# Kernel optimization log

Measured on AMD Instinct MI355X. Metric: run time of the kernel, lower is better.

Reference implementation:

```python
import jax, jax.numpy as jnp
import numpy as np

B, N, C = 4, 2304, 256
H = 8                      # num_heads
D = C // H                 # head_dim = 32
SCALE = D ** -0.5
H_DS, W_DS = 48, 48
UP = 2                     # spatial_down_ratio
EPS = 1e-5


def setup_inputs() -> dict:
    key = jax.random.key(0)
    ks = jax.random.split(key, 16)
    g = lambda k, shape, s: (jax.random.normal(k, shape, dtype=jnp.float32) * s)
    return {
        "x1": g(ks[0], (B, N, C), 1.0),
        "x2": g(ks[1], (B, N, C), 1.0),
        # attention projections (torch Linear convention: [out, in], no bias)
        "q1_w": g(ks[2], (C, C), C ** -0.5),
        "kv1_w": g(ks[3], (2 * C, C), C ** -0.5),
        "q2_w": g(ks[4], (C, C), C ** -0.5),
        "kv2_w": g(ks[5], (2 * C, C), C ** -0.5),
        # per-head scalar biases
        "beta12": jnp.full((H,), 0.2, dtype=jnp.float32),
        "beta21": jnp.full((H,), 0.1, dtype=jnp.float32),
        # output projections
        "p1_w": g(ks[6], (C, C), (2.0 / C) ** 0.5),
        "p1_b": g(ks[7], (C,), 1e-2),
        "p2_w": g(ks[8], (C, C), (2.0 / C) ** 0.5),
        "p2_b": g(ks[9], (C,), 1e-2),
        # LayerNorm affine params
        "g1": jnp.ones((C,), dtype=jnp.float32),
        "b1": jnp.zeros((C,), dtype=jnp.float32),
        "g2": jnp.ones((C,), dtype=jnp.float32),
        "b2": jnp.zeros((C,), dtype=jnp.float32),
    }


def _heads(x):
    # [B,N,C] -> [B,H,N,D]
    return x.reshape(B, N, H, D).transpose(0, 2, 1, 3)


def _merge(x):
    # [B,H,N,D] -> [B,N,C]
    return x.transpose(0, 2, 1, 3).reshape(B, N, C)


def _cross_attn(q, k, v, beta):
    # scores: [B,H,N,N] with per-head scalar bias
    s = jnp.einsum("bhqd,bhkd->bhqk", q, k) * SCALE + beta[None, :, None, None]
    a = jax.nn.softmax(s, axis=-1)
    return jnp.einsum("bhqk,bhkd->bhqd", a, v)


def _layernorm(x, g, b):
    mu = jnp.mean(x, axis=-1, keepdims=True)
    var = jnp.var(x, axis=-1, keepdims=True)
    return (x - mu) * jax.lax.rsqrt(var + EPS) * g + b


def _forward(x1, x2, q1_w, kv1_w, q2_w, kv2_w, beta12, beta21,
             p1_w, p1_b, p2_w, p2_b, g1, b1, g2, b2):
    q1 = _heads(x1 @ q1_w.T)
    kv1 = x1 @ kv1_w.T          # [B,N,2C]
    k1, v1 = _heads(kv1[..., :C]), _heads(kv1[..., C:])
    q2 = _heads(x2 @ q2_w.T)
    kv2 = x2 @ kv2_w.T
    k2, v2 = _heads(kv2[..., :C]), _heads(kv2[..., C:])

    o1 = _merge(_cross_attn(q1, k2, v2, beta12))   # x1 attends to x2
    o2 = _merge(_cross_attn(q2, k1, v1, beta21))   # x2 attends to x1

    y1 = _layernorm(jax.nn.relu(o1 @ p1_w.T + p1_b), g1, b1)
    y2 = _layernorm(jax.nn.relu(o2 @ p2_w.T + p2_b), g2, b2)

    # [B,N,C] -> [B,C,H_ds,W_ds]
    y1 = y1.transpose(0, 2, 1).reshape(B, C, H_DS, W_DS)
    y2 = y2.transpose(0, 2, 1).reshape(B, C, H_DS, W_DS)

    # bilinear upsample x2, align_corners=False (half-pixel == jax.image default)
    out_shape = (B, C, H_DS * UP, W_DS * UP)
    y1 = jax.image.resize(y1, out_shape, method="bilinear")
    y2 = jax.image.resize(y2, out_shape, method="bilinear")
    return y1, y2


def reference(x1, x2, q1_w, kv1_w, q2_w, kv2_w, beta12, beta21,
              p1_w, p1_b, p2_w, p2_b, g1, b1, g2, b2):
    return _forward(x1, x2, q1_w, kv1_w, q2_w, kv2_w, beta12, beta21,
                    p1_w, p1_b, p2_w, p2_b, g1, b1, g2, b2)
```

## Files before the change

kernel.cpp:

```cpp
#include <hip/hip_runtime.h>
#include <math.h>


typedef __attribute__((ext_vector_type(8))) short short8;
typedef __attribute__((ext_vector_type(4))) float f32x4;
typedef __attribute__((ext_vector_type(16))) float f32x16;
typedef __attribute__((ext_vector_type(2))) unsigned uint32x2;

#define MFMA16(a, b, c) __builtin_amdgcn_mfma_f32_16x16x32_bf16((a), (b), (c), 0, 0, 0)
#define MFMA32(a, b, c) __builtin_amdgcn_mfma_f32_32x32x16_bf16((a), (b), (c), 0, 0, 0)

__device__ __forceinline__ float bf2f(ushort u) {
    union { unsigned u; float f; } x; x.u = ((unsigned)u) << 16; return x.f;
}
__device__ __forceinline__ ushort f2bf(float f) {
    union { float f; unsigned u; } x; x.f = f;
    unsigned u = x.u;
    return (ushort)((u + 0x7fffu + ((u >> 16) & 1u)) >> 16);
}
__device__ __forceinline__ unsigned cvt_pk_bf16(float a, float b) {
    unsigned r;
    asm("v_cvt_pk_bf16_f32 %0, %1, %2" : "=v"(r) : "v"(a), "v"(b));
    return r;
}
__device__ __forceinline__ float fast_ex2(float x) {
    float r;
    asm("v_exp_f32 %0, %1" : "=v"(r) : "v"(x));
    return r;
}
__device__ __forceinline__ void plswap(unsigned &a, unsigned &b) {
    uint32x2 r = __builtin_amdgcn_permlane32_swap(a, b, false, false);
    a = r[0]; b = r[1];
}

__global__ void sniff_kernel(const ushort* __restrict__ x, int* __restrict__ flag)
{
    int lane = threadIdx.x;
    ushort u = x[lane * 2];
    int e = (u >> 7) & 0xFF;
    int outlier = (e < 100 || e > 135) ? 1 : 0;
    unsigned long long m = __ballot(outlier);
    if (lane == 0) *flag = (__popcll(m) >= 16) ? 1 : 0;
}

__global__ __launch_bounds__(256) void convert_params(
    const void* s0, const void* s1, const void* s2, const void* s3,
    const void* s4, const void* s5, const void* s6, const void* s7,
    const void* s8, const void* s9, const void* s10, const void* s11,
    ushort* __restrict__ dst, const int* __restrict__ flag)
{
    int idx = blockIdx.x * 256 + threadIdx.x;
    if (idx >= 525824) return;
    const void* src; int off;
    if      (idx < 65536)  { src = s0;  off = idx; }
    else if (idx < 196608) { src = s1;  off = idx - 65536; }
    else if (idx < 262144) { src = s2;  off = idx - 196608; }
    else if (idx < 393216) { src = s3;  off = idx - 262144; }
    else if (idx < 458752) { src = s4;  off = idx - 393216; }
    else if (idx < 524288) { src = s5;  off = idx - 458752; }
    else if (idx < 524544) { src = s6;  off = idx - 524288; }
    else if (idx < 524800) { src = s7;  off = idx - 524544; }
    else if (idx < 525056) { src = s8;  off = idx - 524800; }
    else if (idx < 525312) { src = s9;  off = idx - 525056; }
    else if (idx < 525568) { src = s10; off = idx - 525312; }
    else                   { src = s11; off = idx - 525568; }
    ushort v = (*flag) ? f2bf(((const float*)src)[off])
                       : ((const ushort*)src)[off];
    dst[idx] = v;
}

__global__ __launch_bounds__(256) void convert_x(
    const void* __restrict__ x1, const void* __restrict__ x2,
    ushort* __restrict__ o1, ushort* __restrict__ o2,
    const int* __restrict__ flag)
{
    int idx = blockIdx.x * 256 + threadIdx.x;
    int which = idx >= 294912;
    int off = (which ? idx - 294912 : idx) * 8;
    const void* src = which ? x2 : x1;
    ushort* dst = which ? o2 : o1;
    if (*flag) {
        const float* p = (const float*)src + off;
        float4 a = *(const float4*)p;
        float4 c = *(const float4*)(p + 4);
        uint4 u;
        u.x = cvt_pk_bf16(a.x, a.y);
        u.y = cvt_pk_bf16(a.z, a.w);
        u.z = cvt_pk_bf16(c.x, c.y);
        u.w = cvt_pk_bf16(c.z, c.w);
        *(uint4*)(dst + off) = u;
    } else {
        *(uint4*)(dst + off) = *(const uint4*)((const ushort*)src + off);
    }
}

__global__ __launch_bounds__(256) void gemm_bt(
    const void* __restrict__ Ain, const ushort* __restrict__ W,
    ushort* __restrict__ C, const ushort* __restrict__ bias,
    int M, int N, int K, int relu, const int* __restrict__ dflag, int a_ext,
    int mode, ushort* __restrict__ Kh, ushort* __restrict__ Vt,
    const ushort* __restrict__ W2, const ushort* __restrict__ bias2,
    ushort* __restrict__ Kh2, ushort* __restrict__ Vt2, int mhalf)
{
    __shared__ __align__(16) ushort As[64][40];
    __shared__ __align__(16) ushort Ws[64][40];

    const int m0 = blockIdx.x * 64;
    const int n0 = blockIdx.y * 64;
    const int tid = threadIdx.x;
    const int w = tid >> 6;
    const int lane = tid & 63;
    const int lm = lane & 15;
    const int quad = lane >> 4;
    const int a32 = a_ext ? *dflag : 0;

    const int side = (mhalf && m0 >= mhalf) ? 1 : 0;
    const ushort* Wu = side ? W2 : W;
    const ushort* bu = side ? bias2 : bias;
    ushort* Khu = side ? Kh2 : Kh;
    ushort* Vtu = side ? Vt2 : Vt;

    const f32x4 Z4 = {0.f, 0.f, 0.f, 0.f};
    f32x4 acc[4];
    for (int j = 0; j < 4; j++) acc[j] = Z4;

    const ushort* A16 = (const ushort*)Ain;
    const float*  A32 = (const float*)Ain;
    const int row = tid >> 2, off = (tid & 3) * 8;

    for (int k0 = 0; k0 < K; k0 += 32) {
        __syncthreads();
        if (a32) {
            const float* p0 = A32 + (size_t)(m0 + row) * K + k0 + off;
            float4 f0 = *(const float4*)p0;
            float4 f1 = *(const float4*)(p0 + 4);
            uint4 t0;
            t0.x = cvt_pk_bf16(f0.x, f0.y);
            t0.y = cvt_pk_bf16(f0.z, f0.w);
            t0.z = cvt_pk_bf16(f1.x, f1.y);
            t0.w = cvt_pk_bf16(f1.z, f1.w);
            *(uint4*)&As[row][off] = t0;
        } else {
            *(uint4*)&As[row][off] =
                *(const uint4*)(A16 + (size_t)(m0 + row) * K + k0 + off);
        }
        *(uint4*)&Ws[row][off] =
            *(const uint4*)(Wu + (size_t)(n0 + row) * K + k0 + off);
        __syncthreads();

        short8 af = *(const short8*)&As[w * 16 + lm][quad * 8];
        for (int nt = 0; nt < 4; nt++) {
            short8 wf = *(const short8*)&Ws[nt * 16 + lm][quad * 8];
            acc[nt] = MFMA16(af, wf, acc[nt]);
        }
    }

    const int grow = m0 + w * 16 + quad * 4;
    const int grel = grow - (side ? mhalf : 0);
    if (mode == 1) {
        const float QSC = 0.17677669529663687f * 1.4426950408889634f;
        int bb = grel / 2304;
        int tok = grel - bb * 2304;
        for (int nt = 0; nt < 4; nt++) {
            int col = n0 + nt * 16 + lm;
            if (col < 256) {
                for (int r = 0; r < 4; r++)
                    C[(size_t)(grow + r) * 256 + col] = f2bf(acc[nt][r] * QSC);
            } else if (col < 512) {
                int c2 = col - 256, hh = c2 >> 5, d = c2 & 31;
                size_t kb = ((size_t)(bb * 8 + hh) * 72 + (tok >> 5)) * 1024
                          + (size_t)(d >> 4) * 512 + (size_t)(d & 15);
                for (int r = 0; r < 4; r++)
                    Khu[kb + (size_t)((tok + r) & 31) * 16] = f2bf(acc[nt][r]);
            } else {
                int c2 = col - 512, hh = c2 >> 5, d = c2 & 31;
                size_t vb = ((size_t)(bb * 8 + hh) * 144 + (tok >> 4)) * 512
                          + (size_t)d * 16 + (size_t)(tok & 15);
                uint2 o;
                o.x = cvt_pk_bf16(acc[nt][0], acc[nt][1]);
                o.y = cvt_pk_bf16(acc[nt][2], acc[nt][3]);
                *(uint2*)&Vtu[vb] = o;
            }
        }
    } else {
        for (int nt = 0; nt < 4; nt++) {
            int col = n0 + nt * 16 + lm;
            float bv = bu ? bf2f(bu[col]) : 0.f;
            for (int r = 0; r < 4; r++) {
                float v = acc[nt][r] + bv;
                if (relu) v = fmaxf(v, 0.f);
                C[(size_t)(grow + r) * N + col] = f2bf(v);
            }
        }
    }
}

__global__ __launch_bounds__(128) void attn_kernel(
    const ushort* __restrict__ Qa, const ushort* __restrict__ Kha,
    const ushort* __restrict__ Vta, ushort* __restrict__ Oa,
    const ushort* __restrict__ Qb, const ushort* __restrict__ Khb2,
    const ushort* __restrict__ Vtb2, ushort* __restrict__ Ob)
{
    const int sid = blockIdx.x;
    const int qb = blockIdx.y;
    const int side = sid >> 5;
    const int bh = sid & 31;
    const ushort* Q  = side ? Qb   : Qa;
    const ushort* Kh = side ? Khb2 : Kha;
    const ushort* Vt = side ? Vtb2 : Vta;
    ushort* O        = side ? Ob   : Oa;

    const int b = bh >> 3, h = bh & 7;
    const int tid = threadIdx.x;
    const int w = tid >> 6, lane = tid & 63;
    const int l31 = lane & 31, hl = lane >> 5;

    const int qrow0 = qb * 128 + w * 64 + l31;
    const int qrow1 = qrow0 + 32;
    const ushort* qp0 = Q + ((size_t)b * 2304 + qrow0) * 256 + h * 32 + hl * 8;
    const ushort* qp1 = Q + ((size_t)b * 2304 + qrow1) * 256 + h * 32 + hl * 8;
    const short8 qf0a = *(const short8*)qp0;
    const short8 qf1a = *(const short8*)(qp0 + 16);
    const short8 qf0b = *(const short8*)qp1;
    const short8 qf1b = *(const short8*)(qp1 + 16);

    f32x16 oa, ob;
    #pragma unroll
    for (int i = 0; i < 16; i++) { oa[i] = 0.f; ob[i] = 0.f; }
    const f32x16 Z16 = oa;
    float la = 0.f, lb = 0.f;

    const ushort* kp0 = Kh + (size_t)bh * 73728 + l31 * 16 + hl * 8;
    const ushort* vp0 = Vt + (size_t)bh * 73728 + l31 * 16 + hl * 8;

#define LOADT(kf0v, kf1v, vf0v, vf1v, t) { \
    const ushort* _kp = kp0 + (size_t)(t) * 1024; \
    kf0v = *(const short8*)_kp; \
    kf1v = *(const short8*)(_kp + 512); \
    const ushort* _vp = vp0 + (size_t)(t) * 1024; \
    vf0v = *(const short8*)_vp; \
    vf1v = *(const short8*)(_vp + 512); \
}
#define QSET(kf0v, kf1v, vf0v, vf1v, qf0v, qf1v, oacc, lacc) { \
    f32x16 s = MFMA32(kf0v, qf0v, Z16); \
    s = MFMA32(kf1v, qf1v, s); \
    float p[16]; \
    _Pragma("unroll") \
    for (int i = 0; i < 16; i++) p[i] = fast_ex2(s[i]); \
    lacc += (((p[0] + p[1]) + (p[2] + p[3])) + ((p[4] + p[5]) + (p[6] + p[7]))) \
          + (((p[8] + p[9]) + (p[10] + p[11])) + ((p[12] + p[13]) + (p[14] + p[15]))); \
    unsigned c0 = cvt_pk_bf16(p[0],  p[1]); \
    unsigned c1 = cvt_pk_bf16(p[2],  p[3]); \
    unsigned c2 = cvt_pk_bf16(p[4],  p[5]); \
    unsigned c3 = cvt_pk_bf16(p[6],  p[7]); \
    unsigned c4 = cvt_pk_bf16(p[8],  p[9]); \
    unsigned c5 = cvt_pk_bf16(p[10], p[11]); \
    unsigned c6 = cvt_pk_bf16(p[12], p[13]); \
    unsigned c7 = cvt_pk_bf16(p[14], p[15]); \
    plswap(c0, c2); plswap(c1, c3); plswap(c4, c6); plswap(c5, c7); \
    union { unsigned u[4]; short8 s8; } pA, pB; \
    pA.u[0] = c0; pA.u[1] = c1; pA.u[2] = c2; pA.u[3] = c3; \
    pB.u[0] = c4; pB.u[1] = c5; pB.u[2] = c6; pB.u[3] = c7; \
    oacc = MFMA32(vf0v, pA.s8, oacc); \
    oacc = MFMA32(vf1v, pB.s8, oacc); \
}
#define COMP(kf0v, kf1v, vf0v, vf1v) { \
    QSET(kf0v, kf1v, vf0v, vf1v, qf0a, qf1a, oa, la); \
    QSET(kf0v, kf1v, vf0v, vf1v, qf0b, qf1b, ob, lb); \
}

    short8 kA0, kA1, vA0, vA1;
    short8 kB0, kB1, vB0, vB1;

    LOADT(kA0, kA1, vA0, vA1, 0);
    LOADT(kB0, kB1, vB0, vB1, 1);

    for (int t = 0; t < 72; t += 2) {
        COMP(kA0, kA1, vA0, vA1);
        { int ta = t + 2 < 72 ? t + 2 : 70; LOADT(kA0, kA1, vA0, vA1, ta); }
        COMP(kB0, kB1, vB0, vB1);
        { int tb = t + 3 < 72 ? t + 3 : 71; LOADT(kB0, kB1, vB0, vB1, tb); }
    }
#undef LOADT
#undef QSET
#undef COMP

    la += __shfl_xor(la, 32, 64);
    lb += __shfl_xor(lb, 32, 64);
    float ra = 1.f / la, rb = 1.f / lb;
    ushort* op0 = O + ((size_t)b * 2304 + qrow0) * 256 + h * 32 + hl * 4;
    ushort* op1 = O + ((size_t)b * 2304 + qrow1) * 256 + h * 32 + hl * 4;
    #pragma unroll
    for (int g = 0; g < 4; g++) {
        uint2 o;
        o.x = cvt_pk_bf16(oa[4 * g] * ra, oa[4 * g + 1] * ra);
        o.y = cvt_pk_bf16(oa[4 * g + 2] * ra, oa[4 * g + 3] * ra);
        *(uint2*)(op0 + 8 * g) = o;
        uint2 o2;
        o2.x = cvt_pk_bf16(ob[4 * g] * rb, ob[4 * g + 1] * rb);
        o2.y = cvt_pk_bf16(ob[4 * g + 2] * rb, ob[4 * g + 3] * rb);
        *(uint2*)(op1 + 8 * g) = o2;
    }
}

__global__ __launch_bounds__(256) void lnt_kernel(
    const ushort* __restrict__ Z, const ushort* __restrict__ G1,
    const ushort* __restrict__ B1, const ushort* __restrict__ G2,
    const ushort* __restrict__ B2, ushort* __restrict__ Yt)
{
    __shared__ ushort T[256][72];

    const int tid = threadIdx.x;
    const int tok0 = blockIdx.x * 32;
    const int half = (tok0 >= 9216) ? 1 : 0;
    const int tr = tok0 - half * 9216;
    const int bb = tr / 2304;
    const int tokb = tr - bb * 2304;

    const int tok_l = tid >> 3;
    const int cq = tid & 7;

    const ushort* zp = Z + ((size_t)(tok0 + tok_l)) * 256 + cq * 32;
    uint dd[16];
    for (int i = 0; i < 4; i++) {
        uint4 v = *(const uint4*)(zp + i * 8);
        dd[i * 4 + 0] = v.x; dd[i * 4 + 1] = v.y;
        dd[i * 4 + 2] = v.z; dd[i * 4 + 3] = v.w;
    }
    float s = 0.f, q = 0.f;
    for (int e = 0; e < 16; e++) {
        float x0 = bf2f((ushort)dd[e]);
        float x1 = bf2f((ushort)(dd[e] >> 16));
        s += x0 + x1;
        q += x0 * x0 + x1 * x1;
    }
    s += __shfl_xor(s, 1, 64); q += __shfl_xor(q, 1, 64);
    s += __shfl_xor(s, 2, 64); q += __shfl_xor(q, 2, 64);
    s += __shfl_xor(s, 4, 64); q += __shfl_xor(q, 4, 64);
    float mu = s * (1.f / 256.f);
    float var = q * (1.f / 256.f) - mu * mu;
    float rs = rsqrtf(var + 1e-5f);

    const ushort* Gs = half ? G2 : G1;
    const ushort* Bs = half ? B2 : B1;
    const int col = tok_l + 4 * cq;

    for (int i = 0; i < 4; i++) {
        int cb = cq * 32 + i * 8;
        uint4 gv = *(const uint4*)(Gs + cb);
        uint4 bv = *(const uint4*)(Bs + cb);
        uint gg[4] = {gv.x, gv.y, gv.z, gv.w};
        uint bw[4] = {bv.x, bv.y, bv.z, bv.w};
        for (int k = 0; k < 4; k++) {
            uint u = dd[i * 4 + k];
            float x0 = bf2f((ushort)u), x1 = bf2f((ushort)(u >> 16));
            float y0 = (x0 - mu) * rs * bf2f((ushort)gg[k]) + bf2f((ushort)bw[k]);
            float y1 = (x1 - mu) * rs * bf2f((ushort)(gg[k] >> 16))
                     + bf2f((ushort)(bw[k] >> 16));
            int c = cb + 2 * k;
            T[c][col]     = f2bf(y0);
            T[c + 1][col] = f2bf(y1);
        }
    }
    __syncthreads();

    const int c_row = tid >> 3;
    const int tq = (tid & 7) * 4;
    const size_t obase = ((size_t)((half * 4 + bb) * 256)) * 2304 + tokb + tq;
    for (int i = 0; i < 8; i++) {
        int c = c_row + 32 * i;
        uint2 v = *(const uint2*)&T[c][tq + 4 * i];
        *(uint2*)(Yt + obase + (size_t)c * 2304) = v;
    }
}

__global__ __launch_bounds__(256) void upsample_kernel(
    const ushort* __restrict__ Yt, float* __restrict__ out)
{
    int idx = blockIdx.x * 256 + threadIdx.x;
    int m  = idx % 48;
    int t  = idx / 48;
    int oi = t % 96;
    int bc = t / 96;

    float fi = oi * 0.5f - 0.25f;
    int i0 = (int)floorf(fi);
    float wi = fi - (float)i0;
    int i1 = i0 + 1 < 47 ? i0 + 1 : 47;
    i0 = i0 > 0 ? i0 : 0;
    int jm = m - 1 > 0 ? m - 1 : 0;
    int jp = m + 1 < 47 ? m + 1 : 47;

    const ushort* r0 = Yt + (size_t)bc * 2304 + i0 * 48;
    const ushort* r1 = Yt + (size_t)bc * 2304 + i1 * 48;
    float a0 = bf2f(r0[jm]), b0 = bf2f(r0[m]), c0 = bf2f(r0[jp]);
    float a1 = bf2f(r1[jm]), b1 = bf2f(r1[m]), c1 = bf2f(r1[jp]);
    float u = 1.f - wi;
    float ha = u * a0 + wi * a1;
    float hb = u * b0 + wi * b1;
    float hc = u * c0 + wi * c1;
    float2 o;
    o.x = 0.25f * ha + 0.75f * hb;
    o.y = 0.75f * hb + 0.25f * hc;
    *(float2*)(out + (size_t)bc * 9216 + oi * 96 + m * 2) = o;
}

extern "C" void kernel_launch(void* const* d_in, const int* in_sizes, int n_in,
                              void* d_out, int out_size, void* d_ws, size_t ws_size,
                              hipStream_t stream)
{
    (void)in_sizes; (void)n_in; (void)out_size; (void)ws_size;

    ushort* ws  = (ushort*)d_ws;
    ushort* Q1  = ws;
    ushort* Q2  = Q1  + 2359296;
    ushort* KV1 = Q2  + 2359296;
    ushort* KV2 = KV1 + 4718592;
    ushort* wc  = KV2 + 4718592;
    int*    dflag = (int*)(wc + 525824);

    ushort* cqkv1w = wc;
    ushort* cqkv2w = wc + 196608;
    ushort* cp1w  = wc + 393216;
    ushort* cp2w  = wc + 458752;
    ushort* cp1b  = wc + 524288;
    ushort* cp2b  = wc + 524544;
    ushort* cg1   = wc + 524800;
    ushort* cb1   = wc + 525056;
    ushort* cg2   = wc + 525312;
    ushort* cb2   = wc + 525568;

    float*  outf = (float*)d_out;
    ushort* O1  = (ushort*)d_out;
    ushort* O2  = O1 + 2359296;
    ushort* Xb1 = O2 + 2359296;
    ushort* Xb2 = Xb1 + 2359296;
    ushort* Z1  = KV2;
    ushort* Yt  = Q1;
    (void)Q2; (void)O2; (void)Xb2;

    dim3 blk(256);
    sniff_kernel<<<dim3(1), dim3(64), 0, stream>>>((const ushort*)d_in[0], dflag);
    convert_params<<<dim3(2054), blk, 0, stream>>>(
        d_in[2], d_in[3], d_in[4], d_in[5], d_in[8], d_in[10],
        d_in[9], d_in[11], d_in[12], d_in[13], d_in[14], d_in[15],
        wc, dflag);
    convert_x<<<dim3(2304), blk, 0, stream>>>(d_in[0], d_in[1], Xb1, Xb2, dflag);

    gemm_bt<<<dim3(288, 12), blk, 0, stream>>>(Xb1, cqkv1w, Q1, nullptr,
        18432, 768, 256, 0, dflag, 0, 1, KV1, KV1 + 2359296,
        cqkv2w, nullptr, KV2, KV2 + 2359296, 9216);

    attn_kernel<<<dim3(64, 18), dim3(128), 0, stream>>>(
        Q1, KV2, KV2 + 2359296, O1,
        Q2, KV1, KV1 + 2359296, O2);

    gemm_bt<<<dim3(288, 4), blk, 0, stream>>>(O1, cp1w, Z1, cp1b,
        18432, 256, 256, 1, dflag, 0, 0, nullptr, nullptr,
        cp2w, cp2b, nullptr, nullptr, 9216);

    lnt_kernel<<<dim3(576), blk, 0, stream>>>(Z1, cg1, cb1, cg2, cb2, Yt);

    upsample_kernel<<<dim3(36864), blk, 0, stream>>>(Yt, outf);
}
```

Baseline: 284.3 us.

## Split attention KV loop across four waves and reduce partials in LDS

The attention kernel now uses 256-thread blocks, doubling the grid along the query dimension. Each block covers 64 query rows, and its four waves each process a quarter (18 tiles) of the KV sequence. Partial outputs and row sums are written to shared memory and then summed by two waves before normalisation and store. This raises the number of concurrent waves for the latency-bound attention loop, at the cost of an LDS reduction, a block barrier and more shared memory per block.

```diff
diff --git a/kernel.cpp b/kernel.cpp
--- a/kernel.cpp
+++ b/kernel.cpp
@@ -195,12 +195,15 @@
     }
 }
 
-__global__ __launch_bounds__(128) void attn_kernel(
+__global__ __launch_bounds__(256) void attn_kernel(
     const ushort* __restrict__ Qa, const ushort* __restrict__ Kha,
     const ushort* __restrict__ Vta, ushort* __restrict__ Oa,
     const ushort* __restrict__ Qb, const ushort* __restrict__ Khb2,
     const ushort* __restrict__ Vtb2, ushort* __restrict__ Ob)
 {
+    __shared__ float Lo[4][2][64][16];
+    __shared__ float Ll[4][2][64];
+
     const int sid = blockIdx.x;
     const int qb = blockIdx.y;
     const int side = sid >> 5;
@@ -215,7 +218,7 @@
     const int w = tid >> 6, lane = tid & 63;
     const int l31 = lane & 31, hl = lane >> 5;
 
-    const int qrow0 = qb * 128 + w * 64 + l31;
+    const int qrow0 = qb * 64 + l31;
     const int qrow1 = qrow0 + 32;
     const ushort* qp0 = Q + ((size_t)b * 2304 + qrow0) * 256 + h * 32 + hl * 8;
     const ushort* qp1 = Q + ((size_t)b * 2304 + qrow1) * 256 + h * 32 + hl * 8;
@@ -272,14 +275,18 @@
     short8 kA0, kA1, vA0, vA1;
     short8 kB0, kB1, vB0, vB1;
 
-    LOADT(kA0, kA1, vA0, vA1, 0);
-    LOADT(kB0, kB1, vB0, vB1, 1);
-
-    for (int t = 0; t < 72; t += 2) {
+    const int t0 = w * 18;
+
+    LOADT(kA0, kA1, vA0, vA1, t0);
+    LOADT(kB0, kB1, vB0, vB1, t0 + 1);
+
+    for (int i = 0; i < 9; i++) {
         COMP(kA0, kA1, vA0, vA1);
-        { int ta = t + 2 < 72 ? t + 2 : 70; LOADT(kA0, kA1, vA0, vA1, ta); }
+        { int ta = t0 + 2 * i + 2; ta = ta < 72 ? ta : 70;
+          LOADT(kA0, kA1, vA0, vA1, ta); }
         COMP(kB0, kB1, vB0, vB1);
-        { int tb = t + 3 < 72 ? t + 3 : 71; LOADT(kB0, kB1, vB0, vB1, tb); }
+        { int tb = t0 + 2 * i + 3; tb = tb < 72 ? tb : 71;
+          LOADT(kB0, kB1, vB0, vB1, tb); }
     }
 #undef LOADT
 #undef QSET
@@ -287,19 +294,37 @@
 
     la += __shfl_xor(la, 32, 64);
     lb += __shfl_xor(lb, 32, 64);
-    float ra = 1.f / la, rb = 1.f / lb;
-    ushort* op0 = O + ((size_t)b * 2304 + qrow0) * 256 + h * 32 + hl * 4;
-    ushort* op1 = O + ((size_t)b * 2304 + qrow1) * 256 + h * 32 + hl * 4;
+
     #pragma unroll
-    for (int g = 0; g < 4; g++) {
-        uint2 o;
-        o.x = cvt_pk_bf16(oa[4 * g] * ra, oa[4 * g + 1] * ra);
-        o.y = cvt_pk_bf16(oa[4 * g + 2] * ra, oa[4 * g + 3] * ra);
-        *(uint2*)(op0 + 8 * g) = o;
-        uint2 o2;
-        o2.x = cvt_pk_bf16(ob[4 * g] * rb, ob[4 * g + 1] * rb);
-        o2.y = cvt_pk_bf16(ob[4 * g + 2] * rb, ob[4 * g + 3] * rb);
-        *(uint2*)(op1 + 8 * g) = o2;
+    for (int r = 0; r < 16; r++) {
+        Lo[w][0][lane][r] = oa[r];
+        Lo[w][1][lane][r] = ob[r];
+    }
+    Ll[w][0][lane] = la;
+    Ll[w][1][lane] = lb;
+    __syncthreads();
+
+    if (w < 2) {
+        float os[16];
+        #pragma unroll
+        for (int r = 0; r < 16; r++) os[r] = 0.f;
+        float ls = 0.f;
+        #pragma unroll
+        for (int u = 0; u < 4; u++) {
+            ls += Ll[u][w][lane];
+            #pragma unroll
+            for (int r = 0; r < 16; r++) os[r] += Lo[u][w][lane][r];
+        }
+        float rl = 1.f / ls;
+        const int qrow = (w == 0) ? qrow0 : qrow1;
+        ushort* op = O + ((size_t)b * 2304 + qrow) * 256 + h * 32 + hl * 4;
+        #pragma unroll
+        for (int g = 0; g < 4; g++) {
+            uint2 o;
+            o.x = cvt_pk_bf16(os[4 * g] * rl, os[4 * g + 1] * rl);
+            o.y = cvt_pk_bf16(os[4 * g + 2] * rl, os[4 * g + 3] * rl);
+            *(uint2*)(op + 8 * g) = o;
+        }
     }
 }
 
@@ -451,7 +476,7 @@
         18432, 768, 256, 0, dflag, 0, 1, KV1, KV1 + 2359296,
         cqkv2w, nullptr, KV2, KV2 + 2359296, 9216);
 
-    attn_kernel<<<dim3(64, 18), dim3(128), 0, stream>>>(
+    attn_kernel<<<dim3(64, 36), dim3(256), 0, stream>>>(
         Q1, KV2, KV2 + 2359296, O1,
         Q2, KV1, KV1 + 2359296, O2);
 
```

Result: faster. 247.2 us (-13.1%).
